# Performance work log

Measured on AMD Instinct MI355X. Metric: run time of the kernel, lower is better.

Reference implementation:

```python
import math
import jax, jax.numpy as jnp
import numpy as np

_INIT_LOG_GAIN = math.log(5.0)
B, L, D = 4, 1024, 256


def setup_inputs() -> dict:
    key = jax.random.key(0)
    kq, kk = jax.random.split(key)
    q = jax.random.normal(kq, (B, L, D), dtype=jnp.float32)
    k = jax.random.normal(kk, (B, L, D), dtype=jnp.float32)
    P_prev = jnp.zeros((B, D, D), dtype=jnp.float32)
    log_gain = jnp.full((D,), _INIT_LOG_GAIN, dtype=jnp.float32)
    output_scale = jnp.ones((D,), dtype=jnp.float32)
    return {"q": q, "k": k, "P_prev": P_prev, "log_gain": log_gain,
            "output_scale": output_scale}


def reference(q, k, P_prev, log_gain, output_scale):
    """Sequential rank-1 projection-state update + normalized matvec + gated tanh.

    q, k: [B, L, D]; P_prev: [B, D, D]. Returns (q_out [B,L,D], P_final [B,D,D]).
    """
    gain = jnp.exp(log_gain)  # effective gain, [D]

    def step(P, qk_t):
        q_t, k_t = qk_t                                   # each [B, D]
        P = P + jnp.einsum('bi,bj->bij', k_t, k_t)        # rank-1 update
        fro = jnp.sqrt(jnp.sum(P * P, axis=(-2, -1), keepdims=True))
        P_norm = P / (fro + 1e-7)
        q_aligned = jnp.einsum('bij,bj->bi', P_norm, q_t)
        q_safe = jnp.tanh(gain * q_aligned) * output_scale
        return P, q_safe

    # scan over the L time axis
    P_final, outs = jax.lax.scan(step, P_prev,
                                 (jnp.swapaxes(q, 0, 1), jnp.swapaxes(k, 0, 1)))
    q_out = jnp.swapaxes(outs, 0, 1)  # [B, L, D]
    return q_out, P_final
```

## Files before the change

### kernel.cpp

```cpp
#include <hip/hip_runtime.h>
#include <math.h>


typedef __attribute__((ext_vector_type(8))) short bf16x8;
typedef __attribute__((ext_vector_type(4))) float f32x4;

__device__ __forceinline__ unsigned short f2bf(float x) {
    union { float f; unsigned u; } c; c.f = x;
    return (unsigned short)((c.u + (0x7fffu + ((c.u >> 16) & 1u))) >> 16);
}
__device__ __forceinline__ unsigned f2bf2(float a, float b) {
    union { float f; unsigned u; } ca, cb; ca.f = a; cb.f = b;
    unsigned ua = ca.u + (0x7fffu + ((ca.u >> 16) & 1u));
    unsigned ub = cb.u + (0x7fffu + ((cb.u >> 16) & 1u));
    return (ua >> 16) | (ub & 0xffff0000u);
}
__device__ __forceinline__ float bf2f(unsigned short h) {
    union { unsigned u; float f; } c; c.u = ((unsigned)h) << 16; return c.f;
}
__device__ __forceinline__ void gload16(const void* g, const void* l) {
    __builtin_amdgcn_global_load_lds(
        (const __attribute__((address_space(1))) unsigned int*)g,
        (__attribute__((address_space(3))) unsigned int*)l, 16, 0, 0);
}
__device__ __forceinline__ bf16x8 ldsfrag(const unsigned short* lds, int row0, int g0, int lane) {
    int r = row0 + (lane & 15);
    int g = g0 + (lane >> 4);
    return *(const bf16x8*)(lds + r * 64 + (((g ^ (r & 7)) & 7) << 3));
}
__device__ __forceinline__ bf16x8 ldsfragf32(const char* tile, int row0, int lane) {
    int r = row0 + (lane & 15);
    int g0 = (lane >> 4) << 1;
    float4 a = *(const float4*)(tile + r * 128 + (((g0 ^ (r & 7)) & 7) << 4));
    float4 b = *(const float4*)(tile + r * 128 + ((((g0 + 1) ^ (r & 7)) & 7) << 4));
    union { unsigned u[4]; bf16x8 v; } o;
    o.u[0] = f2bf2(a.x, a.y); o.u[1] = f2bf2(a.z, a.w);
    o.u[2] = f2bf2(b.x, b.y); o.u[3] = f2bf2(b.z, b.w);
    return o.v;
}
#define MFMA16(a, b, c) __builtin_amdgcn_mfma_f32_16x16x32_bf16(a, b, c, 0, 0, 0)

__global__ __launch_bounds__(256) void k_gsp(
    const float* __restrict__ Q, const float* __restrict__ K,
    const float* __restrict__ Pprev,
    unsigned short* __restrict__ Sc, float* __restrict__ r2d,
    unsigned short* __restrict__ KThi, unsigned short* __restrict__ KTlo,
    float* __restrict__ basePart,
    int B_, int L, int D, int nT, int nPairs)
{
    __shared__ char smem[49152];
    int tid = threadIdx.x, lane = tid & 63, w = tid >> 6;
    int fr = lane & 15, fq = lane >> 4;
    int nDt = D >> 6, nLt = L >> 6;
    int nGS = B_ * nPairs;
    int nKT = B_ * nLt * nDt;
    int bx = blockIdx.x;
    int id = (bx < nGS) ? ((bx & 7) * (nGS >> 3) + (bx >> 3)) : bx;

    if (id < nGS) {
        int p = id % nPairs;
        int b = id / nPairs;
        int ti = (int)((sqrtf(8.f * p + 1.f) - 1.f) * 0.5f);
        while ((ti + 1) * (ti + 2) / 2 <= p) ti++;
        while (ti * (ti + 1) / 2 > p) ti--;
        int sj = p - ti * (ti + 1) / 2;

        const float* Qf = Q + (size_t)b * L * D;
        const float* Kf = K + (size_t)b * L * D;
        int t0 = ti * 64, s0 = sj * 64;
        int wr = w >> 1, wc = w & 1;

        f32x4 g00 = {0,0,0,0}, g01 = {0,0,0,0}, g10 = {0,0,0,0}, g11 = {0,0,0,0};
        f32x4 s00 = {0,0,0,0}, s01 = {0,0,0,0}, s10 = {0,0,0,0}, s11 = {0,0,0,0};

        auto STAGE = [&](int ck, int bo) {
            const float* Kt = Kf + (size_t)t0 * D + ck * 32;
            const float* Qt = Qf + (size_t)t0 * D + ck * 32;
            const float* Ks = Kf + (size_t)s0 * D + ck * 32;
            for (int c = w; c < 8; c += 4) {
                int lrow = c * 8 + (lane >> 3);
                int gof = lrow * D + ((((lane & 7) ^ (lrow & 7)) & 7) << 2);
                gload16(Kt + gof, smem + bo + c * 1024);
                gload16(Qt + gof, smem + bo + 8192 + c * 1024);
                gload16(Ks + gof, smem + bo + 16384 + c * 1024);
            }
        };

        STAGE(0, 0);
        __syncthreads();
        for (int ck = 0; ck < 8; ck++) {
            int cur = (ck & 1) * 24576;
            if (ck < 7) STAGE(ck + 1, 24576 - cur);
            const char* Kt = smem + cur;
            const char* Qt = Kt + 8192;
            const char* Ks = Kt + 16384;
            bf16x8 bK0 = ldsfragf32(Ks, wc * 32, lane);
            bf16x8 bK1 = ldsfragf32(Ks, wc * 32 + 16, lane);
            bf16x8 aK0 = ldsfragf32(Kt, wr * 32, lane);
            bf16x8 aK1 = ldsfragf32(Kt, wr * 32 + 16, lane);
            bf16x8 aQ0 = ldsfragf32(Qt, wr * 32, lane);
            bf16x8 aQ1 = ldsfragf32(Qt, wr * 32 + 16, lane);
            g00 = MFMA16(aK0, bK0, g00);
            g01 = MFMA16(aK0, bK1, g01);
            g10 = MFMA16(aK1, bK0, g10);
            g11 = MFMA16(aK1, bK1, g11);
            s00 = MFMA16(aQ0, bK0, s00);
            s01 = MFMA16(aQ0, bK1, s01);
            s10 = MFMA16(aQ1, bK0, s10);
            s11 = MFMA16(aQ1, bK1, s11);
            __syncthreads();
        }

        float rsv[2][4] = {{0, 0, 0, 0}, {0, 0, 0, 0}};
        unsigned short* sb = (unsigned short*)smem;
#define EPI(MI, NI, AG, AS) { _Pragma("unroll") \
        for (int reg = 0; reg < 4; reg++) { \
            int tl = wr * 32 + MI * 16 + fq * 4 + reg; \
            int sl2 = wc * 32 + NI * 16 + fr; \
            int t = ti * 64 + tl, s = sj * 64 + sl2; \
            float g = AG[reg]; \
            float wgt = (s < t) ? 2.f : (s == t ? 1.f : 0.f); \
            rsv[MI][reg] += wgt * g * g; \
            sb[tl * 64 + sl2] = f2bf((s <= t) ? AS[reg] : 0.f); \
        } }
        EPI(0, 0, g00, s00) EPI(0, 1, g01, s01)
        EPI(1, 0, g10, s10) EPI(1, 1, g11, s11)
#undef EPI
        __syncthreads();
        {
            unsigned short* ScT = Sc + ((size_t)(b * nPairs + p) << 12);
            const uint4* s4 = (const uint4*)sb;
            uint4* d4 = (uint4*)ScT;
            d4[tid] = s4[tid];
            d4[tid + 256] = s4[tid + 256];
        }
#pragma unroll
        for (int off = 1; off < 16; off <<= 1) {
#pragma unroll
            for (int mi = 0; mi < 2; mi++)
#pragma unroll
                for (int reg = 0; reg < 4; reg++)
                    rsv[mi][reg] += __shfl_xor(rsv[mi][reg], off);
        }
        if (fr == 0) {
#pragma unroll
            for (int mi = 0; mi < 2; mi++)
#pragma unroll
                for (int reg = 0; reg < 4; reg++) {
                    int t = ti * 64 + wr * 32 + mi * 16 + fq * 4 + reg;
                    r2d[((size_t)(b * 2 * nT) + sj * 2 + wc) * L + t] = rsv[mi][reg];
                }
        }
    } else if (id < nGS + nKT) {
        int id2 = id - nGS;
        int dt = id2 % nDt, lt = (id2 / nDt) % nLt, b = id2 / (nDt * nLt);
        int l0 = lt * 64, d0 = dt * 64;
        const float* Kf = K + (size_t)b * L * D;
        unsigned short* KThp = KThi + (size_t)b * D * L;
        unsigned short* KTlp = KTlo + (size_t)b * D * L;
        float* lds = (float*)smem;
        int r = tid >> 2, cq = (tid & 3) << 4;
#pragma unroll
        for (int i = 0; i < 16; i += 4) {
            float4 kv = *(const float4*)(Kf + (size_t)(l0 + r) * D + d0 + cq + i);
            lds[r * 65 + cq + i] = kv.x;     lds[r * 65 + cq + i + 1] = kv.y;
            lds[r * 65 + cq + i + 2] = kv.z; lds[r * 65 + cq + i + 3] = kv.w;
        }
        __syncthreads();
        int d2 = tid >> 2, cl = (tid & 3) << 4;
#pragma unroll
        for (int i = 0; i < 16; i += 2) {
            float v0 = lds[(cl + i) * 65 + d2];
            float v1 = lds[(cl + i + 1) * 65 + d2];
            unsigned short h0 = f2bf(v0), h1 = f2bf(v1);
            size_t off = (size_t)(d0 + d2) * L + l0 + cl + i;
            *(unsigned*)(KThp + off) = (unsigned)h0 | ((unsigned)h1 << 16);
            *(unsigned*)(KTlp + off) = f2bf2(v0 - bf2f(h0), v1 - bf2f(h1));
        }
    } else {
        int id2 = id - nGS - nKT;
        int n = D * D / 16;
        const float* P = Pprev + (size_t)(id2 >> 4) * D * D + (size_t)(id2 & 15) * n;
        float* lds = (float*)smem;
        float s = 0.f;
        for (int i = tid * 4; i < n; i += 1024) {
            float4 vv = *(const float4*)(P + i);
            s += vv.x * vv.x + vv.y * vv.y + vv.z * vv.z + vv.w * vv.w;
        }
#pragma unroll
        for (int off = 32; off; off >>= 1) s += __shfl_down(s, off);
        if (lane == 0) lds[w] = s;
        __syncthreads();
        if (tid == 0) basePart[id2] = lds[0] + lds[1] + lds[2] + lds[3];
    }
}

__global__ __launch_bounds__(256) void k_scan(
    const float* __restrict__ K, const float* __restrict__ Pprev,
    const float* __restrict__ r2d, const float* __restrict__ basePart,
    float* __restrict__ invfro, int B_, int L, int D, int nT)
{
    __shared__ float wred[4];
    int b = blockIdx.x;
    int tid = threadIdx.x, lane = tid & 63, w = tid >> 6;
    float bb = 0.f;
#pragma unroll
    for (int i = 0; i < 16; i++) bb += basePart[b * 16 + i];

    int t0v = tid * 4;
    int ns = 2 * ((t0v >> 6) + 1);
    float4 vs = {0.f, 0.f, 0.f, 0.f};
    for (int j = 0; j < ns; j++) {
        float4 rr = *(const float4*)&r2d[((size_t)(b * 2 * nT) + j) * L + t0v];
        vs.x += rr.x; vs.y += rr.y; vs.z += rr.z; vs.w += rr.w;
    }
    float v[4] = {vs.x, vs.y, vs.z, vs.w};
    if (bb != 0.f) {
#pragma unroll
        for (int u2 = 0; u2 < 4; u2++) {
            int t = t0v + u2;
            const float* kt = K + ((size_t)b * L + t) * D;
            const float* P = Pprev + (size_t)b * D * D;
            float c = 0.f;
            for (int i = 0; i < D; i++) {
                float a2 = 0.f;
                for (int j2 = 0; j2 < D; j2++) a2 += P[i * D + j2] * kt[j2];
                c += kt[i] * a2;
            }
            v[u2] += 2.f * c;
        }
    }
    v[1] += v[0]; v[2] += v[1]; v[3] += v[2];
    float tot = v[3], sc2 = tot;
    for (int off = 1; off < 64; off <<= 1) {
        float n2 = __shfl_up(sc2, off);
        if (lane >= off) sc2 += n2;
    }
    if (lane == 63) wred[w] = sc2;
    __syncthreads();
    float woff = 0.f;
    for (int i2 = 0; i2 < w; i2++) woff += wred[i2];
    float exc = woff + sc2 - tot;
#pragma unroll
    for (int u2 = 0; u2 < 4; u2++)
        invfro[(size_t)b * L + t0v + u2] = 1.f / (sqrtf(bb + exc + v[u2]) + 1e-7f);
}

__global__ __launch_bounds__(256) void k_yp(
    const float* __restrict__ Q,
    const float* __restrict__ Pprev, const float* __restrict__ log_gain,
    const float* __restrict__ oscale,
    const unsigned short* __restrict__ Sc, const float* __restrict__ invfro,
    const unsigned short* __restrict__ KThi, const unsigned short* __restrict__ KTlo,
    const float* __restrict__ basePart,
    float* __restrict__ out, float* __restrict__ outP,
    int B_, int L, int D, int nT, int nPairs)
{
    __shared__ unsigned short ys[18432];
    __shared__ float invf[1024];
    int tid = threadIdx.x, lane = tid & 63, w = tid >> 6;
    int fr = lane & 15, fq = lane >> 4;
    int nDh = 16;
    int nY = B_ * (nT >> 1) * nDh;
    int bx = blockIdx.x;
    int id = (bx < nY) ? ((bx & 7) * (nY >> 3) + (bx >> 3)) : bx;

    if (id < nY) {
        int dh = id % nDh;
        int u = (id / nDh) % (nT >> 1);
        int b = id / (nDh * (nT >> 1));
        int d0 = dh * 16;

        float bb = 0.f;
#pragma unroll
        for (int i = 0; i < 16; i++) bb += basePart[b * 16 + i];
        *(float4*)&invf[tid * 4] = *(const float4*)&invfro[(size_t)b * L + tid * 4];
        __syncthreads();

        int twl = w << 4;
        int ti0 = u, ti1 = nT - 1 - u;
        int pb0 = ti0 * (ti0 + 1) / 2, pb1 = ti1 * (ti1 + 1) / 2;
        const unsigned short* ScB = Sc + ((size_t)b * nPairs << 12);
        const unsigned short* KTb = KThi + (size_t)b * D * L;

        f32x4 c0 = {0, 0, 0, 0};
        f32x4 c1 = {0, 0, 0, 0};

        auto STAGE = [&](int sj, int bo) {
            const unsigned short* T1p = ScB + ((size_t)(pb1 + sj) << 12);
            if (sj <= u) {
                const unsigned short* T0p = ScB + ((size_t)(pb0 + sj) << 12);
                for (int c = w; c < 8; c += 4) {
                    int lrow = c * 8 + (lane >> 3);
                    int go = lrow * 64 + ((((lane & 7) ^ (lrow & 7)) & 7) << 3);
                    gload16(T0p + go, ys + bo + c * 512);
                }
            }
            for (int c = w; c < 8; c += 4) {
                int lrow = c * 8 + (lane >> 3);
                int go = lrow * 64 + ((((lane & 7) ^ (lrow & 7)) & 7) << 3);
                gload16(T1p + go, ys + bo + 4096 + c * 512);
            }
            if (w < 2) {
                int lrow = w * 8 + (lane >> 3);
                int gsw = (((lane & 7) ^ (lrow & 7)) & 7) << 3;
                gload16(KTb + (size_t)(d0 + lrow) * L + sj * 64 + gsw,
                        ys + bo + 8192 + w * 512);
            }
        };

        STAGE(0, 0);
        __syncthreads();
        for (int sj = 0; sj <= ti1; sj++) {
            int cur = (sj & 1) * 9216;
            if (sj < ti1) STAGE(sj + 1, 9216 - cur);
            const unsigned short* S0 = ys + cur;
            const unsigned short* S1 = S0 + 4096;
            const unsigned short* KTl = S0 + 8192;
#pragma unroll
            for (int kc = 0; kc < 2; kc++) {
                bf16x8 b0 = ldsfrag(KTl, 0, kc * 4, lane);
                bf16x8 A1 = ldsfrag(S1, twl, kc * 4, lane);
                c1 = MFMA16(A1, b0, c1);
                if (sj <= ti0) {
                    bf16x8 A0 = ldsfrag(S0, twl, kc * 4, lane);
                    c0 = MFMA16(A0, b0, c0);
                }
            }
            __syncthreads();
        }

        if (bb != 0.f) {
            const float* Qf = Q + (size_t)b * L * D;
            const float* Pb = Pprev + (size_t)b * D * D;
            for (int jj = 0; jj < D; jj++) {
                float p0 = Pb[(size_t)(d0 + fr) * D + jj];
#pragma unroll
                for (int reg = 0; reg < 4; reg++) {
                    float q0v = Qf[(size_t)(ti0 * 64 + twl + fq * 4 + reg) * D + jj];
                    float q1v = Qf[(size_t)(ti1 * 64 + twl + fq * 4 + reg) * D + jj];
                    c0[reg] += q0v * p0;
                    c1[reg] += q1v * p0;
                }
            }
        }

        float gg0 = expf(log_gain[d0 + fr]), os0 = oscale[d0 + fr];
        float* outb = out + (size_t)b * L * D;
#pragma unroll
        for (int reg = 0; reg < 4; reg++) {
            int t0 = ti0 * 64 + twl + fq * 4 + reg;
            int t1 = ti1 * 64 + twl + fq * 4 + reg;
            outb[(size_t)t0 * D + d0 + fr] = tanhf(gg0 * c0[reg] * invf[t0]) * os0;
            outb[(size_t)t1 * D + d0 + fr] = tanhf(gg0 * c1[reg] * invf[t1]) * os0;
        }
    } else {
        int id2 = id - nY;
        int b = id2 >> 4, ij = id2 & 15;
        int i0 = (ij >> 2) << 6, j0 = (ij & 3) << 6;
        const unsigned short* Hb = KThi + (size_t)b * D * L;
        const unsigned short* Lb = KTlo + (size_t)b * D * L;
        int wr = w >> 1, wc = w & 1;
        unsigned short* Ah = ys;
        unsigned short* Al = ys + 4096;
        unsigned short* Bh = ys + 8192;
        unsigned short* Bl = ys + 12288;

        f32x4 c00 = {0,0,0,0}, c01 = {0,0,0,0}, c10 = {0,0,0,0}, c11 = {0,0,0,0};
        for (int ck = 0; ck < 16; ck++) {
            __syncthreads();
            for (int c = w; c < 8; c += 4) {
                int lrow = c * 8 + (lane >> 3);
                int gof = (((lane & 7) ^ (lrow & 7)) & 7) << 3;
                gload16(Hb + (size_t)(i0 + lrow) * L + ck * 64 + gof, Ah + c * 512);
                gload16(Lb + (size_t)(i0 + lrow) * L + ck * 64 + gof, Al + c * 512);
                gload16(Hb + (size_t)(j0 + lrow) * L + ck * 64 + gof, Bh + c * 512);
                gload16(Lb + (size_t)(j0 + lrow) * L + ck * 64 + gof, Bl + c * 512);
            }
            __syncthreads();
#pragma unroll
            for (int kc = 0; kc < 2; kc++) {
                bf16x8 ah0 = ldsfrag(Ah, wr * 32, kc * 4, lane);
                bf16x8 ah1 = ldsfrag(Ah, wr * 32 + 16, kc * 4, lane);
                bf16x8 al0 = ldsfrag(Al, wr * 32, kc * 4, lane);
                bf16x8 al1 = ldsfrag(Al, wr * 32 + 16, kc * 4, lane);
                bf16x8 bh0 = ldsfrag(Bh, wc * 32, kc * 4, lane);
                bf16x8 bh1 = ldsfrag(Bh, wc * 32 + 16, kc * 4, lane);
                bf16x8 bl0 = ldsfrag(Bl, wc * 32, kc * 4, lane);
                bf16x8 bl1 = ldsfrag(Bl, wc * 32 + 16, kc * 4, lane);
                c00 = MFMA16(ah0, bh0, c00); c00 = MFMA16(ah0, bl0, c00); c00 = MFMA16(al0, bh0, c00);
                c01 = MFMA16(ah0, bh1, c01); c01 = MFMA16(ah0, bl1, c01); c01 = MFMA16(al0, bh1, c01);
                c10 = MFMA16(ah1, bh0, c10); c10 = MFMA16(ah1, bl0, c10); c10 = MFMA16(al1, bh0, c10);
                c11 = MFMA16(ah1, bh1, c11); c11 = MFMA16(ah1, bl1, c11); c11 = MFMA16(al1, bh1, c11);
            }
        }
        const float* Pb = Pprev + (size_t)b * D * D;
        float* Ob = outP + (size_t)b * D * D;
#define PEPI(MI, NI, ACC) { _Pragma("unroll") \
        for (int reg = 0; reg < 4; reg++) { \
            int i = i0 + wr * 32 + MI * 16 + fq * 4 + reg; \
            int j = j0 + wc * 32 + NI * 16 + fr; \
            Ob[(size_t)i * D + j] = Pb[(size_t)i * D + j] + ACC[reg]; \
        } }
        PEPI(0, 0, c00) PEPI(0, 1, c01) PEPI(1, 0, c10) PEPI(1, 1, c11)
#undef PEPI
    }
}

extern "C" void kernel_launch(void* const* d_in, const int* in_sizes, int n_in,
                              void* d_out, int out_size, void* d_ws, size_t ws_size,
                              hipStream_t stream) {
    const float* q = (const float*)d_in[0];
    const float* k = (const float*)d_in[1];
    const float* Pprev = (const float*)d_in[2];
    const float* log_gain = (const float*)d_in[3];
    const float* oscale = (const float*)d_in[4];

    int D = in_sizes[3];
    int B = in_sizes[2] / (D * D);
    int L = in_sizes[0] / (B * D);
    int nT = L / 64;
    int nPairs = nT * (nT + 1) / 2;
    int nDt = D >> 6;
    int nLt = L >> 6;

    if (D != 256 || L != 1024) return;

    float* out = (float*)d_out;
    float* outP = out + (size_t)B * L * D;

    size_t sR = (size_t)B * L * 2 * nT;
    size_t sBP = 64;
    size_t sI = (size_t)B * L;
    size_t sSc = (size_t)B * nPairs * 4096;
    size_t sKT = (size_t)B * D * L;
    size_t need = (sR + sBP + sI) * sizeof(float) + (sSc + 2 * sKT) * 2;
    if (ws_size < need) return;

    float* r2d = (float*)d_ws;
    float* basePart = r2d + sR;
    float* invfro = basePart + sBP;
    unsigned short* Sc = (unsigned short*)(invfro + sI);
    unsigned short* KThi = Sc + sSc;
    unsigned short* KTlo = KThi + sKT;

    int grid1 = B * nPairs + B * nLt * nDt + B * 16;
    int grid2 = B * (nT >> 1) * 16 + B * nDt * nDt;

    k_gsp<<<grid1, 256, 0, stream>>>(q, k, Pprev, Sc, r2d, KThi, KTlo, basePart,
                                     B, L, D, nT, nPairs);
    k_scan<<<B, 256, 0, stream>>>(k, Pprev, r2d, basePart, invfro, B, L, D, nT);
    k_yp<<<grid2, 256, 0, stream>>>(q, Pprev, log_gain, oscale, Sc, invfro, KThi, KTlo,
                                    basePart, out, outP, B, L, D, nT, nPairs);
}
```

Before: 50.16 us.

## Pre-convert Q/K to bf16 in a prep kernel before the Gram/score GEMM

Splits the fused kernel into a prep kernel and a GEMM kernel. The prep kernel casts Q and K to bf16 once, alongside the existing transpose and norm work, and the GEMM kernel then stages bf16 tiles directly. This halves the bytes the GEMM loads, cuts LDS use, and removes the repeated per-fragment fp32-to-bf16 conversion inside the MFMA loop, because each K tile is reused by many triangular pairs. In exchange it adds an extra kernel launch, a serial dependency between the two kernels, and extra global writes and reads for the bf16 copies.

```diff
diff --git a/kernel.cpp b/kernel.cpp
--- a/kernel.cpp
+++ b/kernel.cpp
@@ -28,78 +28,125 @@
     int g = g0 + (lane >> 4);
     return *(const bf16x8*)(lds + r * 64 + (((g ^ (r & 7)) & 7) << 3));
 }
-__device__ __forceinline__ bf16x8 ldsfragf32(const char* tile, int row0, int lane) {
-    int r = row0 + (lane & 15);
-    int g0 = (lane >> 4) << 1;
-    float4 a = *(const float4*)(tile + r * 128 + (((g0 ^ (r & 7)) & 7) << 4));
-    float4 b = *(const float4*)(tile + r * 128 + ((((g0 + 1) ^ (r & 7)) & 7) << 4));
-    union { unsigned u[4]; bf16x8 v; } o;
-    o.u[0] = f2bf2(a.x, a.y); o.u[1] = f2bf2(a.z, a.w);
-    o.u[2] = f2bf2(b.x, b.y); o.u[3] = f2bf2(b.z, b.w);
-    return o.v;
-}
 #define MFMA16(a, b, c) __builtin_amdgcn_mfma_f32_16x16x32_bf16(a, b, c, 0, 0, 0)
 
-__global__ __launch_bounds__(256) void k_gsp(
+__global__ __launch_bounds__(256) void k_prep(
     const float* __restrict__ Q, const float* __restrict__ K,
     const float* __restrict__ Pprev,
+    unsigned short* __restrict__ Qb, unsigned short* __restrict__ Kb,
+    unsigned short* __restrict__ KThi, unsigned short* __restrict__ KTlo,
+    float* __restrict__ basePart, int B_, int L, int D)
+{
+    __shared__ float lds[64 * 65];
+    int tid = threadIdx.x, lane = tid & 63, w = tid >> 6;
+    int nDt = D >> 6, nLt = L >> 6;
+    int nC = B_ * nLt * nDt;
+    int id = blockIdx.x;
+    if (id < nC) {
+        int dt = id % nDt, lt = (id / nDt) % nLt, b = id / (nDt * nLt);
+        int l0 = lt * 64, d0 = dt * 64;
+        const float* Qf = Q + (size_t)b * L * D;
+        const float* Kf = K + (size_t)b * L * D;
+        unsigned short* Qbp = Qb + (size_t)b * L * D;
+        unsigned short* Kbp = Kb + (size_t)b * L * D;
+        unsigned short* KThp = KThi + (size_t)b * D * L;
+        unsigned short* KTlp = KTlo + (size_t)b * D * L;
+        int r = tid >> 2, cq = (tid & 3) << 4;
+#pragma unroll
+        for (int i = 0; i < 16; i += 4) {
+            float4 qv = *(const float4*)(Qf + (size_t)(l0 + r) * D + d0 + cq + i);
+            float4 kv = *(const float4*)(Kf + (size_t)(l0 + r) * D + d0 + cq + i);
+            uint2 qo; qo.x = f2bf2(qv.x, qv.y); qo.y = f2bf2(qv.z, qv.w);
+            uint2 ko; ko.x = f2bf2(kv.x, kv.y); ko.y = f2bf2(kv.z, kv.w);
+            *(uint2*)(Qbp + (size_t)(l0 + r) * D + d0 + cq + i) = qo;
+            *(uint2*)(Kbp + (size_t)(l0 + r) * D + d0 + cq + i) = ko;
+            lds[r * 65 + cq + i]     = kv.x; lds[r * 65 + cq + i + 1] = kv.y;
+            lds[r * 65 + cq + i + 2] = kv.z; lds[r * 65 + cq + i + 3] = kv.w;
+        }
+        __syncthreads();
+        int d2 = tid >> 2, cl = (tid & 3) << 4;
+#pragma unroll
+        for (int i = 0; i < 16; i += 2) {
+            float v0 = lds[(cl + i) * 65 + d2];
+            float v1 = lds[(cl + i + 1) * 65 + d2];
+            unsigned short h0 = f2bf(v0), h1 = f2bf(v1);
+            size_t off = (size_t)(d0 + d2) * L + l0 + cl + i;
+            *(unsigned*)(KThp + off) = (unsigned)h0 | ((unsigned)h1 << 16);
+            *(unsigned*)(KTlp + off) = f2bf2(v0 - bf2f(h0), v1 - bf2f(h1));
+        }
+    } else {
+        int id2 = id - nC;
+        int n = D * D / 16;
+        const float* P = Pprev + (size_t)(id2 >> 4) * D * D + (size_t)(id2 & 15) * n;
+        float s = 0.f;
+        for (int i = tid * 4; i < n; i += 1024) {
+            float4 vv = *(const float4*)(P + i);
+            s += vv.x * vv.x + vv.y * vv.y + vv.z * vv.z + vv.w * vv.w;
+        }
+#pragma unroll
+        for (int off = 32; off; off >>= 1) s += __shfl_down(s, off);
+        if (lane == 0) lds[w] = s;
+        __syncthreads();
+        if (tid == 0) basePart[id2] = lds[0] + lds[1] + lds[2] + lds[3];
+    }
+}
+
+__global__ __launch_bounds__(256) void k_gs(
+    const unsigned short* __restrict__ Qb, const unsigned short* __restrict__ Kb,
     unsigned short* __restrict__ Sc, float* __restrict__ r2d,
-    unsigned short* __restrict__ KThi, unsigned short* __restrict__ KTlo,
-    float* __restrict__ basePart,
     int B_, int L, int D, int nT, int nPairs)
 {
-    __shared__ char smem[49152];
+    __shared__ unsigned short smem[24576];
     int tid = threadIdx.x, lane = tid & 63, w = tid >> 6;
     int fr = lane & 15, fq = lane >> 4;
-    int nDt = D >> 6, nLt = L >> 6;
     int nGS = B_ * nPairs;
-    int nKT = B_ * nLt * nDt;
     int bx = blockIdx.x;
-    int id = (bx < nGS) ? ((bx & 7) * (nGS >> 3) + (bx >> 3)) : bx;
-
-    if (id < nGS) {
-        int p = id % nPairs;
-        int b = id / nPairs;
-        int ti = (int)((sqrtf(8.f * p + 1.f) - 1.f) * 0.5f);
-        while ((ti + 1) * (ti + 2) / 2 <= p) ti++;
-        while (ti * (ti + 1) / 2 > p) ti--;
-        int sj = p - ti * (ti + 1) / 2;
-
-        const float* Qf = Q + (size_t)b * L * D;
-        const float* Kf = K + (size_t)b * L * D;
-        int t0 = ti * 64, s0 = sj * 64;
-        int wr = w >> 1, wc = w & 1;
-
-        f32x4 g00 = {0,0,0,0}, g01 = {0,0,0,0}, g10 = {0,0,0,0}, g11 = {0,0,0,0};
-        f32x4 s00 = {0,0,0,0}, s01 = {0,0,0,0}, s10 = {0,0,0,0}, s11 = {0,0,0,0};
-
-        auto STAGE = [&](int ck, int bo) {
-            const float* Kt = Kf + (size_t)t0 * D + ck * 32;
-            const float* Qt = Qf + (size_t)t0 * D + ck * 32;
-            const float* Ks = Kf + (size_t)s0 * D + ck * 32;
-            for (int c = w; c < 8; c += 4) {
-                int lrow = c * 8 + (lane >> 3);
-                int gof = lrow * D + ((((lane & 7) ^ (lrow & 7)) & 7) << 2);
-                gload16(Kt + gof, smem + bo + c * 1024);
-                gload16(Qt + gof, smem + bo + 8192 + c * 1024);
-                gload16(Ks + gof, smem + bo + 16384 + c * 1024);
-            }
-        };
-
-        STAGE(0, 0);
-        __syncthreads();
-        for (int ck = 0; ck < 8; ck++) {
-            int cur = (ck & 1) * 24576;
-            if (ck < 7) STAGE(ck + 1, 24576 - cur);
-            const char* Kt = smem + cur;
-            const char* Qt = Kt + 8192;
-            const char* Ks = Kt + 16384;
-            bf16x8 bK0 = ldsfragf32(Ks, wc * 32, lane);
-            bf16x8 bK1 = ldsfragf32(Ks, wc * 32 + 16, lane);
-            bf16x8 aK0 = ldsfragf32(Kt, wr * 32, lane);
-            bf16x8 aK1 = ldsfragf32(Kt, wr * 32 + 16, lane);
-            bf16x8 aQ0 = ldsfragf32(Qt, wr * 32, lane);
-            bf16x8 aQ1 = ldsfragf32(Qt, wr * 32 + 16, lane);
+    int id = (bx & 7) * (nGS >> 3) + (bx >> 3);
+
+    int p = id % nPairs;
+    int b = id / nPairs;
+    int ti = (int)((sqrtf(8.f * p + 1.f) - 1.f) * 0.5f);
+    while ((ti + 1) * (ti + 2) / 2 <= p) ti++;
+    while (ti * (ti + 1) / 2 > p) ti--;
+    int sj = p - ti * (ti + 1) / 2;
+
+    const unsigned short* Qp = Qb + (size_t)b * L * D;
+    const unsigned short* Kp = Kb + (size_t)b * L * D;
+    int t0 = ti * 64, s0 = sj * 64;
+    int wr = w >> 1, wc = w & 1;
+
+    f32x4 g00 = {0,0,0,0}, g01 = {0,0,0,0}, g10 = {0,0,0,0}, g11 = {0,0,0,0};
+    f32x4 s00 = {0,0,0,0}, s01 = {0,0,0,0}, s10 = {0,0,0,0}, s11 = {0,0,0,0};
+
+    auto STAGE = [&](int ck, int bo) {
+        const unsigned short* Kt = Kp + (size_t)t0 * D + ck * 64;
+        const unsigned short* Qt = Qp + (size_t)t0 * D + ck * 64;
+        const unsigned short* Ks = Kp + (size_t)s0 * D + ck * 64;
+        for (int c = w; c < 8; c += 4) {
+            int lrow = c * 8 + (lane >> 3);
+            int gof = lrow * D + ((((lane & 7) ^ (lrow & 7)) & 7) << 3);
+            gload16(Kt + gof, smem + bo + c * 512);
+            gload16(Qt + gof, smem + bo + 4096 + c * 512);
+            gload16(Ks + gof, smem + bo + 8192 + c * 512);
+        }
+    };
+
+    STAGE(0, 0);
+    __syncthreads();
+    for (int ck = 0; ck < 4; ck++) {
+        int cur = (ck & 1) * 12288;
+        if (ck < 3) STAGE(ck + 1, 12288 - cur);
+        const unsigned short* Kt = smem + cur;
+        const unsigned short* Qt = Kt + 4096;
+        const unsigned short* Ks = Kt + 8192;
+#pragma unroll
+        for (int kc = 0; kc < 2; kc++) {
+            bf16x8 bK0 = ldsfrag(Ks, wc * 32, kc * 4, lane);
+            bf16x8 bK1 = ldsfrag(Ks, wc * 32 + 16, kc * 4, lane);
+            bf16x8 aK0 = ldsfrag(Kt, wr * 32, kc * 4, lane);
+            bf16x8 aK1 = ldsfrag(Kt, wr * 32 + 16, kc * 4, lane);
+            bf16x8 aQ0 = ldsfrag(Qt, wr * 32, kc * 4, lane);
+            bf16x8 aQ1 = ldsfrag(Qt, wr * 32 + 16, kc * 4, lane);
             g00 = MFMA16(aK0, bK0, g00);
             g01 = MFMA16(aK0, bK1, g01);
             g10 = MFMA16(aK1, bK0, g10);
@@ -108,90 +155,48 @@
             s01 = MFMA16(aQ0, bK1, s01);
             s10 = MFMA16(aQ1, bK0, s10);
             s11 = MFMA16(aQ1, bK1, s11);
-            __syncthreads();
-        }
-
-        float rsv[2][4] = {{0, 0, 0, 0}, {0, 0, 0, 0}};
-        unsigned short* sb = (unsigned short*)smem;
+        }
+        __syncthreads();
+    }
+
+    float rsv[2][4] = {{0, 0, 0, 0}, {0, 0, 0, 0}};
 #define EPI(MI, NI, AG, AS) { _Pragma("unroll") \
-        for (int reg = 0; reg < 4; reg++) { \
-            int tl = wr * 32 + MI * 16 + fq * 4 + reg; \
-            int sl2 = wc * 32 + NI * 16 + fr; \
-            int t = ti * 64 + tl, s = sj * 64 + sl2; \
-            float g = AG[reg]; \
-            float wgt = (s < t) ? 2.f : (s == t ? 1.f : 0.f); \
-            rsv[MI][reg] += wgt * g * g; \
-            sb[tl * 64 + sl2] = f2bf((s <= t) ? AS[reg] : 0.f); \
-        } }
-        EPI(0, 0, g00, s00) EPI(0, 1, g01, s01)
-        EPI(1, 0, g10, s10) EPI(1, 1, g11, s11)
+    for (int reg = 0; reg < 4; reg++) { \
+        int tl = wr * 32 + MI * 16 + fq * 4 + reg; \
+        int sl2 = wc * 32 + NI * 16 + fr; \
+        int t = ti * 64 + tl, s = sj * 64 + sl2; \
+        float g = AG[reg]; \
+        float wgt = (s < t) ? 2.f : (s == t ? 1.f : 0.f); \
+        rsv[MI][reg] += wgt * g * g; \
+        smem[tl * 64 + sl2] = f2bf((s <= t) ? AS[reg] : 0.f); \
+    } }
+    EPI(0, 0, g00, s00) EPI(0, 1, g01, s01)
+    EPI(1, 0, g10, s10) EPI(1, 1, g11, s11)
 #undef EPI
-        __syncthreads();
-        {
-            unsigned short* ScT = Sc + ((size_t)(b * nPairs + p) << 12);
-            const uint4* s4 = (const uint4*)sb;
-            uint4* d4 = (uint4*)ScT;
-            d4[tid] = s4[tid];
-            d4[tid + 256] = s4[tid + 256];
-        }
-#pragma unroll
-        for (int off = 1; off < 16; off <<= 1) {
-#pragma unroll
-            for (int mi = 0; mi < 2; mi++)
-#pragma unroll
-                for (int reg = 0; reg < 4; reg++)
-                    rsv[mi][reg] += __shfl_xor(rsv[mi][reg], off);
-        }
-        if (fr == 0) {
-#pragma unroll
-            for (int mi = 0; mi < 2; mi++)
-#pragma unroll
-                for (int reg = 0; reg < 4; reg++) {
-                    int t = ti * 64 + wr * 32 + mi * 16 + fq * 4 + reg;
-                    r2d[((size_t)(b * 2 * nT) + sj * 2 + wc) * L + t] = rsv[mi][reg];
-                }
-        }
-    } else if (id < nGS + nKT) {
-        int id2 = id - nGS;
-        int dt = id2 % nDt, lt = (id2 / nDt) % nLt, b = id2 / (nDt * nLt);
-        int l0 = lt * 64, d0 = dt * 64;
-        const float* Kf = K + (size_t)b * L * D;
-        unsigned short* KThp = KThi + (size_t)b * D * L;
-        unsigned short* KTlp = KTlo + (size_t)b * D * L;
-        float* lds = (float*)smem;
-        int r = tid >> 2, cq = (tid & 3) << 4;
-#pragma unroll
-        for (int i = 0; i < 16; i += 4) {
-            float4 kv = *(const float4*)(Kf + (size_t)(l0 + r) * D + d0 + cq + i);
-            lds[r * 65 + cq + i] = kv.x;     lds[r * 65 + cq + i + 1] = kv.y;
-            lds[r * 65 + cq + i + 2] = kv.z; lds[r * 65 + cq + i + 3] = kv.w;
-        }
-        __syncthreads();
-        int d2 = tid >> 2, cl = (tid & 3) << 4;
-#pragma unroll
-        for (int i = 0; i < 16; i += 2) {
-            float v0 = lds[(cl + i) * 65 + d2];
-            float v1 = lds[(cl + i + 1) * 65 + d2];
-            unsigned short h0 = f2bf(v0), h1 = f2bf(v1);
-            size_t off = (size_t)(d0 + d2) * L + l0 + cl + i;
-            *(unsigned*)(KThp + off) = (unsigned)h0 | ((unsigned)h1 << 16);
-            *(unsigned*)(KTlp + off) = f2bf2(v0 - bf2f(h0), v1 - bf2f(h1));
-        }
-    } else {
-        int id2 = id - nGS - nKT;
-        int n = D * D / 16;
-        const float* P = Pprev + (size_t)(id2 >> 4) * D * D + (size_t)(id2 & 15) * n;
-        float* lds = (float*)smem;
-        float s = 0.f;
-        for (int i = tid * 4; i < n; i += 1024) {
-            float4 vv = *(const float4*)(P + i);
-            s += vv.x * vv.x + vv.y * vv.y + vv.z * vv.z + vv.w * vv.w;
-        }
-#pragma unroll
-        for (int off = 32; off; off >>= 1) s += __shfl_down(s, off);
-        if (lane == 0) lds[w] = s;
-        __syncthreads();
-        if (tid == 0) basePart[id2] = lds[0] + lds[1] + lds[2] + lds[3];
+    __syncthreads();
+    {
+        unsigned short* ScT = Sc + ((size_t)(b * nPairs + p) << 12);
+        const uint4* s4 = (const uint4*)smem;
+        uint4* d4 = (uint4*)ScT;
+        d4[tid] = s4[tid];
+        d4[tid + 256] = s4[tid + 256];
+    }
+#pragma unroll
+    for (int off = 1; off < 16; off <<= 1) {
+#pragma unroll
+        for (int mi = 0; mi < 2; mi++)
+#pragma unroll
+            for (int reg = 0; reg < 4; reg++)
+                rsv[mi][reg] += __shfl_xor(rsv[mi][reg], off);
+    }
+    if (fr == 0) {
+#pragma unroll
+        for (int mi = 0; mi < 2; mi++)
+#pragma unroll
+            for (int reg = 0; reg < 4; reg++) {
+                int t = ti * 64 + wr * 32 + mi * 16 + fq * 4 + reg;
+                r2d[((size_t)(b * 2 * nT) + sj * 2 + wc) * L + t] = rsv[mi][reg];
+            }
     }
 }
 
@@ -433,22 +438,26 @@
     size_t sBP = 64;
     size_t sI = (size_t)B * L;
     size_t sSc = (size_t)B * nPairs * 4096;
+    size_t sLD = (size_t)B * L * D;
     size_t sKT = (size_t)B * D * L;
-    size_t need = (sR + sBP + sI) * sizeof(float) + (sSc + 2 * sKT) * 2;
+    size_t need = (sR + sBP + sI) * sizeof(float) + (sSc + 2 * sLD + 2 * sKT) * 2;
     if (ws_size < need) return;
 
     float* r2d = (float*)d_ws;
     float* basePart = r2d + sR;
     float* invfro = basePart + sBP;
     unsigned short* Sc = (unsigned short*)(invfro + sI);
-    unsigned short* KThi = Sc + sSc;
+    unsigned short* Qb = Sc + sSc;
+    unsigned short* Kb = Qb + sLD;
+    unsigned short* KThi = Kb + sLD;
     unsigned short* KTlo = KThi + sKT;
 
-    int grid1 = B * nPairs + B * nLt * nDt + B * 16;
+    int grid0 = B * nLt * nDt + B * 16;
+    int grid1 = B * nPairs;
     int grid2 = B * (nT >> 1) * 16 + B * nDt * nDt;
 
-    k_gsp<<<grid1, 256, 0, stream>>>(q, k, Pprev, Sc, r2d, KThi, KTlo, basePart,
-                                     B, L, D, nT, nPairs);
+    k_prep<<<grid0, 256, 0, stream>>>(q, k, Pprev, Qb, Kb, KThi, KTlo, basePart, B, L, D);
+    k_gs<<<grid1, 256, 0, stream>>>(Qb, Kb, Sc, r2d, B, L, D, nT, nPairs);
     k_scan<<<B, 256, 0, stream>>>(k, Pprev, r2d, basePart, invfro, B, L, D, nT);
     k_yp<<<grid2, 256, 0, stream>>>(q, Pprev, log_gain, oscale, Sc, invfro, KThi, KTlo,
                                     basePart, out, outP, B, L, D, nT, nPairs);
```

Result: faster. 48.86 us (-2.6%).
